# Kernel tuning notes

Hardware: AMD Instinct MI355X
Metric: run time of the kernel (lower is better)

Reference implementation:

```python
import jax, jax.numpy as jnp
import numpy as np

N_USERS = 100000
N_ITEMS = 50000
DIM = 64
N_EDGES = 4_000_000
NUM_LAYERS = 3


def setup_inputs() -> dict:
    key = jax.random.key(0)
    k1, k2, k3 = jax.random.split(key, 3)
    # xavier_uniform-like scale for embeddings
    scale = float(np.sqrt(6.0 / (N_USERS + DIM)))
    user_emb = jax.random.uniform(k1, (N_USERS, DIM), jnp.float32, -scale, scale)
    scale_i = float(np.sqrt(6.0 / (N_ITEMS + DIM)))
    item_emb = jax.random.uniform(k2, (N_ITEMS, DIM), jnp.float32, -scale_i, scale_i)
    edge_index = jax.random.randint(k3, (2, N_EDGES), 0, N_USERS + N_ITEMS, dtype=jnp.int64)
    return {"user_emb": user_emb, "item_emb": item_emb, "edge_index": edge_index}


def reference(user_emb, item_emb, edge_index):
    """LightGCN_W.encode_window: K rounds of symmetric-normalized SpMM, then layer mean."""
    n_users = user_emb.shape[0]
    n_nodes = n_users + item_emb.shape[0]
    row, col = edge_index[0], edge_index[1]  # messages flow row (source) -> col (target)

    # gcn_norm with add_self_loops=False (PyG LGConv default)
    ones = jnp.ones(row.shape[0], dtype=user_emb.dtype)
    deg = jax.ops.segment_sum(ones, col, num_segments=n_nodes)
    dinv = jnp.where(deg > 0, jax.lax.rsqrt(jnp.maximum(deg, 1e-12)), 0.0)
    norm = (dinv[row] * dinv[col])[:, None]  # [E, 1]

    x = jnp.concatenate([user_emb, item_emb], axis=0)  # [N, D]
    acc = x
    for _ in range(NUM_LAYERS):
        x = jax.ops.segment_sum(norm * x[row], col, num_segments=n_nodes)
        acc = acc + x
    out = acc / (NUM_LAYERS + 1)
    return out[:n_users], out[n_users:]
```

## Files before the change

### kernel.cpp

```cpp
#include <hip/hip_runtime.h>
#include <hip/hip_fp16.h>

#define DIM 64
#define BSH 8
#define BMASK 255u
#define NBMAX 1024
#define BINC 16384
#define BSTRIDE 8192


__global__ void zero_ints(int* __restrict__ p, int n) {
    int i = blockIdx.x * blockDim.x + threadIdx.x;
    if (i < n) p[i] = 0;
}

__global__ __launch_bounds__(1024) void bin_kernel(const int* __restrict__ edge, int E,
                                                   int* __restrict__ bcur,
                                                   unsigned* __restrict__ bin, int NB) {
    __shared__ unsigned stage[BINC];
    __shared__ int lcnt[NBMAX];
    __shared__ int lsc[NBMAX];
    __shared__ int lcur[NBMAX];
    __shared__ int gb[NBMAX];
    const int tid = (int)threadIdx.x;
    const int beg = (int)blockIdx.x * BINC;
    const int n = min(BINC, E - beg);

    lcnt[tid] = 0;
    __syncthreads();
    for (int i = tid; i < n; i += 1024)
        atomicAdd(&lcnt[edge[E + beg + i] >> BSH], 1);
    __syncthreads();
    lsc[tid] = lcnt[tid];
    __syncthreads();
    for (int off = 1; off < 1024; off <<= 1) {
        int t = (tid >= off) ? lsc[tid - off] : 0;
        __syncthreads();
        lsc[tid] += t;
        __syncthreads();
    }
    {
        int cb = lcnt[tid];
        lcur[tid] = lsc[tid] - cb;
        if (tid < NB) gb[tid] = cb ? atomicAdd(&bcur[tid], cb) : 0;
    }
    __syncthreads();
    for (int i = tid; i < n; i += 1024) {
        int r = edge[beg + i];
        int c = edge[E + beg + i];
        int b = c >> BSH;
        int slot = atomicAdd(&lcur[b], 1);
        stage[slot] = ((unsigned)r << BSH) | ((unsigned)c & BMASK);
    }
    __syncthreads();
    const int wid = tid >> 6, lane = tid & 63;
    for (int b = wid; b < NB; b += 16) {
        int cb = lcnt[b];
        if (!cb) continue;
        int lb = lsc[b] - cb;
        int g = b * BSTRIDE + gb[b];
        for (int l = lane; l < cb; l += 64)
            bin[g + l] = stage[lb + l];
    }
}

__global__ __launch_bounds__(256) void csr_kernel(const unsigned* __restrict__ bin,
                                                  const int* __restrict__ bcnt,
                                                  const float* __restrict__ user,
                                                  const float* __restrict__ item,
                                                  int nU,
                                                  int2* __restrict__ pdesc,
                                                  float* __restrict__ dinv,
                                                  float* __restrict__ rdinv,
                                                  int* __restrict__ row_sorted,
                                                  __half* __restrict__ y0,
                                                  int nN) {
    __shared__ int lcnt[256];
    __shared__ int lsc[256];
    __shared__ int lcur[256];
    __shared__ float sdinv[256];
    const int tid = (int)threadIdx.x;
    const int b = (int)blockIdx.x;
    const int abase = b * BSTRIDE;
    const int cnt = bcnt[b];
    lcnt[tid] = 0;
    __syncthreads();
    for (int i = tid; i < cnt; i += 256)
        atomicAdd(&lcnt[bin[abase + i] & BMASK], 1);
    __syncthreads();
    lsc[tid] = lcnt[tid];
    __syncthreads();
    for (int off = 1; off < 256; off <<= 1) {
        int t = (tid >= off) ? lsc[tid - off] : 0;
        __syncthreads();
        lsc[tid] += t;
        __syncthreads();
    }
    const int cb = lcnt[tid];
    const int lb = lsc[tid] - cb;
    lcur[tid] = abase + lb;
    float dv = cb ? rsqrtf((float)cb) : 0.0f;
    sdinv[tid] = dv;
    int node = (b << BSH) + tid;
    if (node < nN) {
        pdesc[node] = make_int2(abase + lb, cb);
        dinv[node] = dv;
        rdinv[node] = cb ? sqrtf((float)cb) : 0.0f;
    }
    __syncthreads();
    for (int i = tid; i < cnt; i += 256) {
        unsigned e = bin[abase + i];
        int c = (int)(e & BMASK);
        int p = atomicAdd(&lcur[c], 1);
        row_sorted[p] = (int)(e >> BSH);
    }
    const int baseNode = b << BSH;
#pragma unroll
    for (int it = 0; it < 8; ++it) {
        int idx = it * 256 + tid;
        int ln = idx >> 3;
        int node2 = baseNode + ln;
        if (node2 < nN) {
            int qc = idx & 7;
            const float* src = (node2 < nU) ? user + (size_t)node2 * DIM
                                            : item + (size_t)(node2 - nU) * DIM;
            float4 e0 = ((const float4*)src)[qc * 2];
            float4 e1 = ((const float4*)src)[qc * 2 + 1];
            float dvn = sdinv[ln];
            float4 pack;
            __half2* p = (__half2*)&pack;
            p[0] = __floats2half2_rn(dvn * e0.x, dvn * e0.y);
            p[1] = __floats2half2_rn(dvn * e0.z, dvn * e0.w);
            p[2] = __floats2half2_rn(dvn * e1.x, dvn * e1.y);
            p[3] = __floats2half2_rn(dvn * e1.z, dvn * e1.w);
            ((float4*)y0)[(size_t)baseNode * 8 + idx] = pack;
        }
    }
}

template<bool LAST>
__global__ __launch_bounds__(256) void layer_kernel(const int2* __restrict__ pdesc,
                                                    const float* __restrict__ dinv,
                                                    const int* __restrict__ row_sorted,
                                                    const __half* __restrict__ y_in,
                                                    __half* __restrict__ y_out,
                                                    const float* __restrict__ user,
                                                    const float* __restrict__ item,
                                                    const float* __restrict__ rdinv,
                                                    const __half* __restrict__ y_prev,
                                                    float* __restrict__ out,
                                                    int nU, int nN) {
    int wave = (int)((blockIdx.x * blockDim.x + threadIdx.x) >> 6);
    int lane = (int)(threadIdx.x & 63);
    if (wave >= nN) return;
    const int2 pd = pdesc[wave];
    const int beg = pd.x;
    const int end = beg + pd.y;
    const int g = lane >> 3;
    const int q = lane & 7;
    const float4* yv = (const float4*)y_in;
    float a0 = 0, a1 = 0, a2 = 0, a3 = 0, a4 = 0, a5 = 0, a6 = 0, a7 = 0;
    const int last = end - 1;
    for (int base = beg; base < end; base += 16) {
        int e0 = base + g;
        int e1 = e0 + 8;
        int i0 = (e0 <= last) ? e0 : last;
        int i1 = (e1 <= last) ? e1 : last;
        float m0 = (e0 <= last) ? 1.0f : 0.0f;
        float m1 = (e1 <= last) ? 1.0f : 0.0f;
        int r0 = row_sorted[i0];
        int r1 = row_sorted[i1];
        float4 v0 = yv[(size_t)r0 * 8 + q];
        float4 v1 = yv[(size_t)r1 * 8 + q];
        const __half2* h0 = (const __half2*)&v0;
        const __half2* h1 = (const __half2*)&v1;
        float2 t;
        t = __half22float2(h0[0]); a0 = fmaf(m0, t.x, a0); a1 = fmaf(m0, t.y, a1);
        t = __half22float2(h0[1]); a2 = fmaf(m0, t.x, a2); a3 = fmaf(m0, t.y, a3);
        t = __half22float2(h0[2]); a4 = fmaf(m0, t.x, a4); a5 = fmaf(m0, t.y, a5);
        t = __half22float2(h0[3]); a6 = fmaf(m0, t.x, a6); a7 = fmaf(m0, t.y, a7);
        t = __half22float2(h1[0]); a0 = fmaf(m1, t.x, a0); a1 = fmaf(m1, t.y, a1);
        t = __half22float2(h1[1]); a2 = fmaf(m1, t.x, a2); a3 = fmaf(m1, t.y, a3);
        t = __half22float2(h1[2]); a4 = fmaf(m1, t.x, a4); a5 = fmaf(m1, t.y, a5);
        t = __half22float2(h1[3]); a6 = fmaf(m1, t.x, a6); a7 = fmaf(m1, t.y, a7);
    }
#pragma unroll
    for (int ofs = 8; ofs <= 32; ofs <<= 1) {
        a0 += __shfl_xor(a0, ofs);
        a1 += __shfl_xor(a1, ofs);
        a2 += __shfl_xor(a2, ofs);
        a3 += __shfl_xor(a3, ofs);
        a4 += __shfl_xor(a4, ofs);
        a5 += __shfl_xor(a5, ofs);
        a6 += __shfl_xor(a6, ofs);
        a7 += __shfl_xor(a7, ofs);
    }
    if (g == 0) {
        float dc = dinv[wave];
        if (!LAST) {
            float s = dc * dc;
            float4 pack;
            __half2* ph = (__half2*)&pack;
            ph[0] = __floats2half2_rn(s * a0, s * a1);
            ph[1] = __floats2half2_rn(s * a2, s * a3);
            ph[2] = __floats2half2_rn(s * a4, s * a5);
            ph[3] = __floats2half2_rn(s * a6, s * a7);
            ((float4*)y_out)[(size_t)wave * 8 + q] = pack;
        } else {
            float rd = rdinv[wave];
            float4 y1r = ((const float4*)y_prev)[(size_t)wave * 8 + q];
            float4 y2r = ((const float4*)y_in)[(size_t)wave * 8 + q];
            const __half2* p1 = (const __half2*)&y1r;
            const __half2* p2 = (const __half2*)&y2r;
            float w[8];
#pragma unroll
            for (int j = 0; j < 4; ++j) {
                float2 u1 = __half22float2(p1[j]);
                float2 u2 = __half22float2(p2[j]);
                w[2 * j]     = u1.x + u2.x;
                w[2 * j + 1] = u1.y + u2.y;
            }
            const float* src = (wave < nU) ? user + (size_t)wave * DIM
                                           : item + (size_t)(wave - nU) * DIM;
            float4 e0 = ((const float4*)src)[q * 2];
            float4 e1 = ((const float4*)src)[q * 2 + 1];
            float4 o0, o1;
            o0.x = 0.25f * (e0.x + rd * w[0] + dc * a0);
            o0.y = 0.25f * (e0.y + rd * w[1] + dc * a1);
            o0.z = 0.25f * (e0.z + rd * w[2] + dc * a2);
            o0.w = 0.25f * (e0.w + rd * w[3] + dc * a3);
            o1.x = 0.25f * (e1.x + rd * w[4] + dc * a4);
            o1.y = 0.25f * (e1.y + rd * w[5] + dc * a5);
            o1.z = 0.25f * (e1.z + rd * w[6] + dc * a6);
            o1.w = 0.25f * (e1.w + rd * w[7] + dc * a7);
            float4* o4 = (float4*)(out + (size_t)wave * DIM + q * 8);
            o4[0] = o0;
            o4[1] = o1;
        }
    }
}


extern "C" void kernel_launch(void* const* d_in, const int* in_sizes, int n_in,
                              void* d_out, int out_size, void* d_ws, size_t ws_size,
                              hipStream_t stream) {
    const float* user = (const float*)d_in[0];
    const float* item = (const float*)d_in[1];
    const int*   edge = (const int*)d_in[2];

    const int nU = in_sizes[0] / DIM;
    const int nI = in_sizes[1] / DIM;
    const int nN = nU + nI;
    const int E  = in_sizes[2] / 2;
    const int NB = (nN + 255) / 256;

    float* out = (float*)d_out;

    char* ws = (char*)d_ws;
    size_t off = 0;
    auto take = [&](size_t bytes) -> char* {
        char* p = ws + off;
        off = (off + bytes + 255) & ~(size_t)255;
        return p;
    };
    const size_t ytab = (size_t)nN * DIM * 2;
    const size_t arena = (size_t)NB * BSTRIDE * 4;
    int*      bcur       = (int*)  take((size_t)NB * 4);
    int2*     pdesc      = (int2*) take((size_t)nN * 8);
    float*    dinv       = (float*)take((size_t)nN * 4);
    float*    rdinv      = (float*)take((size_t)nN * 4);
    int*      row_sorted = (int*)  take(arena);
    char*     R1 = take(arena > ytab ? arena : ytab);
    char*     R2 = take(ytab);
    char*     R3 = take(ytab);
    unsigned* bin = (unsigned*)R1;
    __half*   y1  = (__half*)R1;
    __half*   y0  = (__half*)R2;
    __half*   y2  = (__half*)R3;
    (void)ws_size; (void)n_in; (void)out_size;

    const int B = 256;
    dim3 blk(B);

    zero_ints<<<dim3((NB + B - 1) / B), blk, 0, stream>>>(bcur, NB);
    bin_kernel<<<dim3((E + BINC - 1) / BINC), dim3(1024), 0, stream>>>(edge, E, bcur, bin, NB);
    csr_kernel<<<dim3(NB), blk, 0, stream>>>(bin, bcur, user, item, nU,
                                             pdesc, dinv, rdinv, row_sorted, y0, nN);

    dim3 lgrid((nN + 3) / 4);
    layer_kernel<false><<<lgrid, blk, 0, stream>>>(pdesc, dinv, row_sorted, y0, y1,
                                                   nullptr, nullptr, nullptr, nullptr, nullptr,
                                                   nU, nN);
    layer_kernel<false><<<lgrid, blk, 0, stream>>>(pdesc, dinv, row_sorted, y1, y2,
                                                   nullptr, nullptr, nullptr, nullptr, nullptr,
                                                   nU, nN);
    layer_kernel<true ><<<lgrid, blk, 0, stream>>>(pdesc, dinv, row_sorted, y2, nullptr,
                                                   user, item, rdinv, y1, out,
                                                   nU, nN);
}
```

Measured before the change: 300.2 us.

## Accumulate SpMM gathers in half2 with 4-way unroll, zero-row padding, LDS-staged bins

```diff
diff --git a/kernel.cpp b/kernel.cpp
--- a/kernel.cpp
+++ b/kernel.cpp
@@ -75,6 +75,7 @@
                                                   int* __restrict__ row_sorted,
                                                   __half* __restrict__ y0,
                                                   int nN) {
+    __shared__ unsigned sbin[BSTRIDE];
     __shared__ int lcnt[256];
     __shared__ int lsc[256];
     __shared__ int lcur[256];
@@ -84,9 +85,11 @@
     const int abase = b * BSTRIDE;
     const int cnt = bcnt[b];
     lcnt[tid] = 0;
-    __syncthreads();
     for (int i = tid; i < cnt; i += 256)
-        atomicAdd(&lcnt[bin[abase + i] & BMASK], 1);
+        sbin[i] = bin[abase + i];
+    __syncthreads();
+    for (int i = tid; i < cnt; i += 256)
+        atomicAdd(&lcnt[sbin[i] & BMASK], 1);
     __syncthreads();
     lsc[tid] = lcnt[tid];
     __syncthreads();
@@ -109,7 +112,7 @@
     }
     __syncthreads();
     for (int i = tid; i < cnt; i += 256) {
-        unsigned e = bin[abase + i];
+        unsigned e = sbin[i];
         int c = (int)(e & BMASK);
         int p = atomicAdd(&lcur[c], 1);
         row_sorted[p] = (int)(e >> BSH);
@@ -138,6 +141,15 @@
     }
 }
 
+__global__ void zero_row_kernel(__half* __restrict__ r1, __half* __restrict__ r2,
+                                __half* __restrict__ r3, int nN) {
+    int t = threadIdx.x;
+    size_t o = (size_t)nN * DIM + t;
+    r1[o] = __float2half(0.0f);
+    r2[o] = __float2half(0.0f);
+    r3[o] = __float2half(0.0f);
+}
+
 template<bool LAST>
 __global__ __launch_bounds__(256) void layer_kernel(const int2* __restrict__ pdesc,
                                                     const float* __restrict__ dinv,
@@ -155,56 +167,62 @@
     if (wave >= nN) return;
     const int2 pd = pdesc[wave];
     const int beg = pd.x;
-    const int end = beg + pd.y;
+    const int n = pd.y;
+    const int zrow = nN;
     const int g = lane >> 3;
     const int q = lane & 7;
     const float4* yv = (const float4*)y_in;
-    float a0 = 0, a1 = 0, a2 = 0, a3 = 0, a4 = 0, a5 = 0, a6 = 0, a7 = 0;
-    const int last = end - 1;
-    for (int base = beg; base < end; base += 16) {
-        int e0 = base + g;
-        int e1 = e0 + 8;
-        int i0 = (e0 <= last) ? e0 : last;
-        int i1 = (e1 <= last) ? e1 : last;
-        float m0 = (e0 <= last) ? 1.0f : 0.0f;
-        float m1 = (e1 <= last) ? 1.0f : 0.0f;
-        int r0 = row_sorted[i0];
-        int r1 = row_sorted[i1];
-        float4 v0 = yv[(size_t)r0 * 8 + q];
-        float4 v1 = yv[(size_t)r1 * 8 + q];
+    __half2 acc0 = __float2half2_rn(0.0f);
+    __half2 acc1 = acc0, acc2 = acc0, acc3 = acc0;
+    for (int base = 0; base < n; base += 32) {
+        int s = base + g;
+        int e = beg + s;
+        int i0 = (s      < n) ? row_sorted[e]      : zrow;
+        int i1 = (s + 8  < n) ? row_sorted[e + 8]  : zrow;
+        int i2 = (s + 16 < n) ? row_sorted[e + 16] : zrow;
+        int i3 = (s + 24 < n) ? row_sorted[e + 24] : zrow;
+        float4 v0 = yv[(size_t)i0 * 8 + q];
+        float4 v1 = yv[(size_t)i1 * 8 + q];
+        float4 v2 = yv[(size_t)i2 * 8 + q];
+        float4 v3 = yv[(size_t)i3 * 8 + q];
         const __half2* h0 = (const __half2*)&v0;
         const __half2* h1 = (const __half2*)&v1;
-        float2 t;
-        t = __half22float2(h0[0]); a0 = fmaf(m0, t.x, a0); a1 = fmaf(m0, t.y, a1);
-        t = __half22float2(h0[1]); a2 = fmaf(m0, t.x, a2); a3 = fmaf(m0, t.y, a3);
-        t = __half22float2(h0[2]); a4 = fmaf(m0, t.x, a4); a5 = fmaf(m0, t.y, a5);
-        t = __half22float2(h0[3]); a6 = fmaf(m0, t.x, a6); a7 = fmaf(m0, t.y, a7);
-        t = __half22float2(h1[0]); a0 = fmaf(m1, t.x, a0); a1 = fmaf(m1, t.y, a1);
-        t = __half22float2(h1[1]); a2 = fmaf(m1, t.x, a2); a3 = fmaf(m1, t.y, a3);
-        t = __half22float2(h1[2]); a4 = fmaf(m1, t.x, a4); a5 = fmaf(m1, t.y, a5);
-        t = __half22float2(h1[3]); a6 = fmaf(m1, t.x, a6); a7 = fmaf(m1, t.y, a7);
+        const __half2* h2 = (const __half2*)&v2;
+        const __half2* h3 = (const __half2*)&v3;
+        acc0 = __hadd2(acc0, h0[0]); acc1 = __hadd2(acc1, h0[1]);
+        acc2 = __hadd2(acc2, h0[2]); acc3 = __hadd2(acc3, h0[3]);
+        acc0 = __hadd2(acc0, h1[0]); acc1 = __hadd2(acc1, h1[1]);
+        acc2 = __hadd2(acc2, h1[2]); acc3 = __hadd2(acc3, h1[3]);
+        acc0 = __hadd2(acc0, h2[0]); acc1 = __hadd2(acc1, h2[1]);
+        acc2 = __hadd2(acc2, h2[2]); acc3 = __hadd2(acc3, h2[3]);
+        acc0 = __hadd2(acc0, h3[0]); acc1 = __hadd2(acc1, h3[1]);
+        acc2 = __hadd2(acc2, h3[2]); acc3 = __hadd2(acc3, h3[3]);
     }
 #pragma unroll
     for (int ofs = 8; ofs <= 32; ofs <<= 1) {
-        a0 += __shfl_xor(a0, ofs);
-        a1 += __shfl_xor(a1, ofs);
-        a2 += __shfl_xor(a2, ofs);
-        a3 += __shfl_xor(a3, ofs);
-        a4 += __shfl_xor(a4, ofs);
-        a5 += __shfl_xor(a5, ofs);
-        a6 += __shfl_xor(a6, ofs);
-        a7 += __shfl_xor(a7, ofs);
+        int t0 = __shfl_xor(*reinterpret_cast<int*>(&acc0), ofs);
+        int t1 = __shfl_xor(*reinterpret_cast<int*>(&acc1), ofs);
+        int t2 = __shfl_xor(*reinterpret_cast<int*>(&acc2), ofs);
+        int t3 = __shfl_xor(*reinterpret_cast<int*>(&acc3), ofs);
+        acc0 = __hadd2(acc0, *reinterpret_cast<__half2*>(&t0));
+        acc1 = __hadd2(acc1, *reinterpret_cast<__half2*>(&t1));
+        acc2 = __hadd2(acc2, *reinterpret_cast<__half2*>(&t2));
+        acc3 = __hadd2(acc3, *reinterpret_cast<__half2*>(&t3));
     }
     if (g == 0) {
         float dc = dinv[wave];
+        float2 s0 = __half22float2(acc0);
+        float2 s1 = __half22float2(acc1);
+        float2 s2 = __half22float2(acc2);
+        float2 s3 = __half22float2(acc3);
         if (!LAST) {
             float s = dc * dc;
             float4 pack;
             __half2* ph = (__half2*)&pack;
-            ph[0] = __floats2half2_rn(s * a0, s * a1);
-            ph[1] = __floats2half2_rn(s * a2, s * a3);
-            ph[2] = __floats2half2_rn(s * a4, s * a5);
-            ph[3] = __floats2half2_rn(s * a6, s * a7);
+            ph[0] = __floats2half2_rn(s * s0.x, s * s0.y);
+            ph[1] = __floats2half2_rn(s * s1.x, s * s1.y);
+            ph[2] = __floats2half2_rn(s * s2.x, s * s2.y);
+            ph[3] = __floats2half2_rn(s * s3.x, s * s3.y);
             ((float4*)y_out)[(size_t)wave * 8 + q] = pack;
         } else {
             float rd = rdinv[wave];
@@ -225,14 +243,14 @@
             float4 e0 = ((const float4*)src)[q * 2];
             float4 e1 = ((const float4*)src)[q * 2 + 1];
             float4 o0, o1;
-            o0.x = 0.25f * (e0.x + rd * w[0] + dc * a0);
-            o0.y = 0.25f * (e0.y + rd * w[1] + dc * a1);
-            o0.z = 0.25f * (e0.z + rd * w[2] + dc * a2);
-            o0.w = 0.25f * (e0.w + rd * w[3] + dc * a3);
-            o1.x = 0.25f * (e1.x + rd * w[4] + dc * a4);
-            o1.y = 0.25f * (e1.y + rd * w[5] + dc * a5);
-            o1.z = 0.25f * (e1.z + rd * w[6] + dc * a6);
-            o1.w = 0.25f * (e1.w + rd * w[7] + dc * a7);
+            o0.x = 0.25f * (e0.x + rd * w[0] + dc * s0.x);
+            o0.y = 0.25f * (e0.y + rd * w[1] + dc * s0.y);
+            o0.z = 0.25f * (e0.z + rd * w[2] + dc * s1.x);
+            o0.w = 0.25f * (e0.w + rd * w[3] + dc * s1.y);
+            o1.x = 0.25f * (e1.x + rd * w[4] + dc * s2.x);
+            o1.y = 0.25f * (e1.y + rd * w[5] + dc * s2.y);
+            o1.z = 0.25f * (e1.z + rd * w[6] + dc * s3.x);
+            o1.w = 0.25f * (e1.w + rd * w[7] + dc * s3.y);
             float4* o4 = (float4*)(out + (size_t)wave * DIM + q * 8);
             o4[0] = o0;
             o4[1] = o1;
@@ -263,7 +281,7 @@
         off = (off + bytes + 255) & ~(size_t)255;
         return p;
     };
-    const size_t ytab = (size_t)nN * DIM * 2;
+    const size_t ytab = (size_t)(nN + 1) * DIM * 2;
     const size_t arena = (size_t)NB * BSTRIDE * 4;
     int*      bcur       = (int*)  take((size_t)NB * 4);
     int2*     pdesc      = (int2*) take((size_t)nN * 8);
@@ -286,6 +304,7 @@
     bin_kernel<<<dim3((E + BINC - 1) / BINC), dim3(1024), 0, stream>>>(edge, E, bcur, bin, NB);
     csr_kernel<<<dim3(NB), blk, 0, stream>>>(bin, bcur, user, item, nU,
                                              pdesc, dinv, rdinv, row_sorted, y0, nN);
+    zero_row_kernel<<<dim3(1), dim3(64), 0, stream>>>(y0, y1, y2, nN);
 
     dim3 lgrid((nN + 3) / 4);
     layer_kernel<false><<<lgrid, blk, 0, stream>>>(pdesc, dinv, row_sorted, y0, y1,
```

Measured after the change: 281.6 us. 6.2% less time.
